# Kernel tuning notes

Hardware: AMD Instinct MI355X
Metric: run time of the kernel (lower is better)

Reference implementation:

```python
import jax, jax.numpy as jnp
import numpy as np

N, E, DIN, DOUT = 50000, 800000, 64, 64


def setup_inputs() -> dict:
    key = jax.random.key(0)
    k1, k2, k3, k4, k5 = jax.random.split(key, 5)
    x = jax.random.normal(k1, (N, DIN), dtype=jnp.float32)
    edge_index = jax.random.randint(k2, (2, E), 0, N, dtype=jnp.int64)
    edge_attr = jax.random.uniform(k3, (E,), dtype=jnp.float32)
    # PyG GCNConv params: linear weight (no bias in lin) + conv bias
    W = jax.random.normal(k4, (DIN, DOUT), dtype=jnp.float32) / np.sqrt(DIN)
    b = jax.random.normal(k5, (DOUT,), dtype=jnp.float32) * 0.01
    return {
        "x": x,
        "edge_index": edge_index,
        "edge_attr": edge_attr,
        "return_attention_weights": 0,
        "W": W,
        "b": b,
    }


def reference(x, edge_index, edge_attr, return_attention_weights, W, b):
    # GCNConv(add_self_loops=False, normalize=True), edge_weight = ones.
    # edge_attr / return_attention_weights are unused by the original module.
    n = x.shape[0]
    src, dst = edge_index[0], edge_index[1]
    # in-degree on destination nodes (gcn_norm with ones edge weights)
    deg = jax.ops.segment_sum(jnp.ones_like(src, dtype=x.dtype), dst, num_segments=n)
    dis = jnp.where(deg > 0, jax.lax.rsqrt(jnp.maximum(deg, 1)), jnp.zeros_like(deg))
    norm = dis[src] * dis[dst]  # [E]
    h = x @ W  # [N, DOUT] -- transform before aggregation (in < out would flip, equal here)
    msg = h[src] * norm[:, None]  # [E, DOUT]
    out = jax.ops.segment_sum(msg, dst, num_segments=n) + b  # [N, DOUT]
    return out
```

## Files before the change

### kernel.cpp

```cpp
#include <hip/hip_runtime.h>
#include <stdint.h>


#define CAP   64
#define BSH   7
#define NBMAX 512
#define EPB   4096
#define BCAP  2816

typedef float vf4 __attribute__((ext_vector_type(4)));

__device__ __forceinline__ int probe_is64(const void* eidx, int n_edges, int n_nodes) {
    int lane = threadIdx.x & 63;
    const long long* p = (const long long*)eidx;
    int cnt = n_edges < 64 ? n_edges : 64;
    long long v = p[lane % cnt];
    bool ok = (v >= 0) && (v < (long long)n_nodes);
    return (__ballot(ok) == ~0ull) ? 1 : 0;
}

__device__ __forceinline__ int load_idx(const void* eidx, long long i, int is64) {
    if (is64) return (int)((const long long*)eidx)[i];
    return ((const int*)eidx)[i];
}

__device__ __forceinline__ unsigned short f2bf(float v) {
    unsigned u = __float_as_uint(v);
    unsigned r = (u + 0x7fffu + ((u >> 16) & 1u)) >> 16;
    return (unsigned short)r;
}

__device__ __forceinline__ float bflo(unsigned u) { return __uint_as_float(u << 16); }
__device__ __forceinline__ float bfhi(unsigned u) { return __uint_as_float(u & 0xffff0000u); }

__global__ __launch_bounds__(256) void k_bin(
    const void* eidx, unsigned* __restrict__ tails,
    unsigned* __restrict__ buckets, int n, int ne, int nb)
{
    __shared__ unsigned histo[NBMAX];
    __shared__ unsigned base[NBMAX];
    const int tid = (int)threadIdx.x;
    for (int i = tid; i < NBMAX; i += 256) histo[i] = 0u;
    int is64 = probe_is64(eidx, ne, n);
    __syncthreads();

    unsigned pk[16], rk[16];
    long long e0 = (long long)blockIdx.x * EPB + tid;
    #pragma unroll
    for (int j = 0; j < 16; ++j) {
        long long e = e0 + 256 * j;
        if (e < (long long)ne) {
            int s = load_idx(eidx, e, is64);
            int t = load_idx(eidx, (long long)ne + e, is64);
            pk[j] = ((unsigned)t << 16) | (unsigned)s;
            rk[j] = atomicAdd(&histo[(unsigned)t >> BSH], 1u);
        } else { pk[j] = 0u; rk[j] = 0xFFFFFFFFu; }
    }
    __syncthreads();
    unsigned U = tails[NBMAX];
    for (int b2 = tid; b2 < nb; b2 += 256) {
        unsigned cc = histo[b2];
        base[b2] = cc ? (atomicAdd(&tails[b2], cc) - U) : 0u;
    }
    __syncthreads();
    #pragma unroll
    for (int j = 0; j < 16; ++j) {
        if (rk[j] != 0xFFFFFFFFu) {
            unsigned bk = pk[j] >> (16 + BSH);
            unsigned slot = base[bk] + rk[j];
            if (slot < (unsigned)BCAP)
                buckets[(size_t)bk * BCAP + slot] = pk[j];
        }
    }
}

__global__ __launch_bounds__(256) void k_gemm(
    const float* __restrict__ x, const float* __restrict__ W,
    unsigned* __restrict__ h32w, int n)
{
    __shared__ float Ws[64 * 64];
    __shared__ float xs[64 * 68];
    const int tid = (int)threadIdx.x;
    const int row0 = (int)blockIdx.x * 64;

    for (int j = 0; j < 4; ++j) {
        int q = tid + 256 * j;
        float4 w4 = ((const float4*)W)[q];
        float* d = &Ws[q * 4];
        d[0] = w4.x; d[1] = w4.y; d[2] = w4.z; d[3] = w4.w;
    }
    for (int j = 0; j < 4; ++j) {
        int q = tid + 256 * j;
        int r = q >> 4, c4 = (q & 15) * 4;
        int row = row0 + r;
        float4 v4 = (row < n) ? ((const float4*)x)[(size_t)row * 16 + (q & 15)]
                              : make_float4(0.f, 0.f, 0.f, 0.f);
        float* d = &xs[r * 68 + c4];
        d[0] = v4.x; d[1] = v4.y; d[2] = v4.z; d[3] = v4.w;
    }
    __syncthreads();

    const int fg = tid & 15, rg = tid >> 4;
    const int r0 = rg * 4;
    float acc[4][4];
    #pragma unroll
    for (int i = 0; i < 4; ++i)
        #pragma unroll
        for (int j = 0; j < 4; ++j) acc[i][j] = 0.f;

    #pragma unroll 4
    for (int k = 0; k < 64; ++k) {
        vf4 w4 = *(const vf4*)&Ws[k * 64 + fg * 4];
        float x0 = xs[(r0 + 0) * 68 + k];
        float x1 = xs[(r0 + 1) * 68 + k];
        float x2 = xs[(r0 + 2) * 68 + k];
        float x3 = xs[(r0 + 3) * 68 + k];
        acc[0][0] += x0 * w4.x; acc[0][1] += x0 * w4.y; acc[0][2] += x0 * w4.z; acc[0][3] += x0 * w4.w;
        acc[1][0] += x1 * w4.x; acc[1][1] += x1 * w4.y; acc[1][2] += x1 * w4.z; acc[1][3] += x1 * w4.w;
        acc[2][0] += x2 * w4.x; acc[2][1] += x2 * w4.y; acc[2][2] += x2 * w4.z; acc[2][3] += x2 * w4.w;
        acc[3][0] += x3 * w4.x; acc[3][1] += x3 * w4.y; acc[3][2] += x3 * w4.z; acc[3][3] += x3 * w4.w;
    }
    #pragma unroll
    for (int i = 0; i < 4; ++i) {
        int row = row0 + r0 + i;
        if (row < n) {
            h32w[(size_t)row * 32 + fg * 2] =
                (unsigned)f2bf(acc[i][0]) | ((unsigned)f2bf(acc[i][1]) << 16);
            h32w[(size_t)row * 32 + fg * 2 + 1] =
                (unsigned)f2bf(acc[i][2]) | ((unsigned)f2bf(acc[i][3]) << 16);
        }
    }
}

__global__ __launch_bounds__(256) void k_place2(
    const unsigned* __restrict__ tails,
    const unsigned* __restrict__ buckets,
    unsigned short* __restrict__ csr16,
    float* __restrict__ dis, unsigned char* __restrict__ endc, int n)
{
    __shared__ unsigned degL[1 << BSH];
    const int tid = (int)threadIdx.x;
    const int b = (int)blockIdx.x;
    const int t0 = b << BSH;
    if (tid < (1 << BSH)) degL[tid] = 0u;
    __syncthreads();
    unsigned U = tails[NBMAX];
    unsigned cnt = tails[b] - U;
    if (cnt > (unsigned)BCAP) cnt = (unsigned)BCAP;
    for (unsigned i = (unsigned)tid; i < cnt; i += 256) {
        unsigned p = buckets[(size_t)b * BCAP + i];
        unsigned dl = (p >> 16) & ((1u << BSH) - 1);
        unsigned r = atomicAdd(&degL[dl], 1u);
        if (r < (unsigned)CAP)
            csr16[((size_t)(t0 + (int)dl)) * CAP + r] = (unsigned short)(p & 0xFFFFu);
    }
    __syncthreads();
    if (tid < (1 << BSH)) {
        int node = t0 + tid;
        if (node < n) {
            unsigned d = degL[tid];
            dis[node] = d ? rsqrtf((float)d) : 0.f;
            endc[node] = (unsigned char)(d < (unsigned)CAP ? d : (unsigned)CAP);
        }
    }
}

__global__ __launch_bounds__(256) void k_place_direct(
    const void* eidx, unsigned* __restrict__ deg,
    unsigned short* __restrict__ csr16, int n, int ne)
{
    int is64 = probe_is64(eidx, ne, n);
    unsigned base = deg[n];
    int e = (int)blockIdx.x * 256 + (int)threadIdx.x;
    if (e >= ne) return;
    int s = load_idx(eidx, e, is64);
    int t = load_idx(eidx, (long long)ne + e, is64);
    unsigned r = atomicAdd(&deg[t], 1u) - base;
    if (r < (unsigned)CAP)
        csr16[(size_t)t * CAP + r] = (unsigned short)s;
}

__global__ __launch_bounds__(256) void k_finalize_direct(
    const unsigned* __restrict__ deg,
    float* __restrict__ dis, unsigned char* __restrict__ endc, int n)
{
    int i = (int)blockIdx.x * 256 + (int)threadIdx.x;
    if (i >= n) return;
    unsigned base = deg[n];
    unsigned cnt = deg[i] - base;
    dis[i] = cnt ? rsqrtf((float)cnt) : 0.f;
    endc[i] = (unsigned char)(cnt < (unsigned)CAP ? cnt : (unsigned)CAP);
}

__global__ __launch_bounds__(256) void k_aggregate(
    const float* __restrict__ dis,
    const unsigned char* __restrict__ endc,
    const unsigned short* __restrict__ csr16,
    const uint2* __restrict__ h64,
    const float* __restrict__ bias,
    float* __restrict__ out, int n)
{
    int wid  = (int)threadIdx.x >> 6;
    int lane = (int)threadIdx.x & 63;
    int t = (int)blockIdx.x * 4 + wid;
    if (t >= n) return;
    int allsrc = (int)csr16[(size_t)t * CAP + lane];
    unsigned end = endc[t];
    float dis_t = dis[t];
    int f = lane & 15, q = lane >> 4;
    float a0 = 0.f, a1 = 0.f, a2 = 0.f, a3 = 0.f;

    unsigned K4 = end >> 4;
    for (unsigned k = 0; k < K4; ++k) {
        int j = q + (int)(k << 4);
        int s0 = __shfl(allsrc, j, 64);
        int s1 = __shfl(allsrc, j + 4, 64);
        int s2 = __shfl(allsrc, j + 8, 64);
        int s3 = __shfl(allsrc, j + 12, 64);
        float w0 = dis[s0], w1 = dis[s1], w2 = dis[s2], w3 = dis[s3];
        uint2 u0 = h64[(size_t)s0 * 16 + f];
        uint2 u1 = h64[(size_t)s1 * 16 + f];
        uint2 u2 = h64[(size_t)s2 * 16 + f];
        uint2 u3 = h64[(size_t)s3 * 16 + f];
        a0 += w0 * bflo(u0.x) + w1 * bflo(u1.x) + w2 * bflo(u2.x) + w3 * bflo(u3.x);
        a1 += w0 * bfhi(u0.x) + w1 * bfhi(u1.x) + w2 * bfhi(u2.x) + w3 * bfhi(u3.x);
        a2 += w0 * bflo(u0.y) + w1 * bflo(u1.y) + w2 * bflo(u2.y) + w3 * bflo(u3.y);
        a3 += w0 * bfhi(u0.y) + w1 * bfhi(u1.y) + w2 * bfhi(u2.y) + w3 * bfhi(u3.y);
    }
    unsigned rem = end & 15u;
    if (rem) {
        unsigned jb = K4 << 4;
        for (unsigned k = 0; k < 4; ++k) {
            unsigned jj = jb + (k << 2) + (unsigned)q;
            bool valid = jj < end;
            int s = __shfl(allsrc, (int)(jj & 63u), 64);
            s = valid ? s : 0;
            float w = valid ? dis[s] : 0.f;
            uint2 u = h64[(size_t)s * 16 + f];
            a0 += w * bflo(u.x);
            a1 += w * bfhi(u.x);
            a2 += w * bflo(u.y);
            a3 += w * bfhi(u.y);
        }
    }
    a0 += __shfl_xor(a0, 16, 64); a0 += __shfl_xor(a0, 32, 64);
    a1 += __shfl_xor(a1, 16, 64); a1 += __shfl_xor(a1, 32, 64);
    a2 += __shfl_xor(a2, 16, 64); a2 += __shfl_xor(a2, 32, 64);
    a3 += __shfl_xor(a3, 16, 64); a3 += __shfl_xor(a3, 32, 64);
    if (q == 0) {
        float4 bb = ((const float4*)bias)[f];
        float4 o;
        o.x = a0 * dis_t + bb.x;
        o.y = a1 * dis_t + bb.y;
        o.z = a2 * dis_t + bb.z;
        o.w = a3 * dis_t + bb.w;
        ((float4*)out)[(size_t)t * 16 + f] = o;
    }
}

extern "C" void kernel_launch(void* const* d_in, const int* in_sizes, int n_in,
                              void* d_out, int out_size, void* d_ws, size_t ws_size,
                              hipStream_t stream) {
    const float* x   = (const float*)d_in[0];
    const void* eidx = d_in[1];
    const float* W   = (const float*)d_in[4];
    const float* b   = (const float*)d_in[5];
    float* out       = (float*)d_out;

    const int n  = in_sizes[0] / 64;
    const int ne = in_sizes[2];
    const int nb = (n + (1 << BSH) - 1) >> BSH;
    const int nchunks = (ne + EPB - 1) / EPB;

    auto al = [](size_t v) { return (v + 255) & ~(size_t)255; };

    size_t need = al((size_t)(NBMAX + 1) * 4) + al((size_t)nb * BCAP * 4)
                + al((size_t)n * CAP * 2) + al((size_t)n * 32 * 4)
                + al((size_t)n * 4) + al((size_t)n);
    bool binned = (ws_size >= need) && (nb <= NBMAX);

    char* base = (char*)d_ws;
    size_t off = 0;
    unsigned*       tails   = (unsigned*)(base + off);       off = al(off + (size_t)(NBMAX + 1) * 4);
    unsigned*       buckets = (unsigned*)(base + off);       off = al(off + (size_t)nb * BCAP * 4);
    unsigned short* csr16   = (unsigned short*)(base + off); off = al(off + (size_t)n * CAP * 2);
    unsigned*       h32     = (unsigned*)(base + off);       off = al(off + (size_t)n * 32 * 4);
    float*          dis     = (float*)(base + off);          off = al(off + (size_t)n * 4);
    unsigned char*  endc    = (unsigned char*)(base + off);  off = al(off + (size_t)n);

    if (binned) {
        k_bin<<<nchunks, 256, 0, stream>>>(eidx, tails, buckets, n, ne, nb);
        k_gemm<<<(n + 63) / 64, 256, 0, stream>>>(x, W, h32, n);
        k_place2<<<nb, 256, 0, stream>>>(tails, buckets, csr16, dis, endc, n);
    } else {
        unsigned* deg = buckets;
        k_gemm<<<(n + 63) / 64, 256, 0, stream>>>(x, W, h32, n);
        k_place_direct<<<(ne + 255) / 256, 256, 0, stream>>>(eidx, deg, csr16, n, ne);
        k_finalize_direct<<<(n + 255) / 256, 256, 0, stream>>>(deg, dis, endc, n);
    }
    k_aggregate<<<(n + 3) / 4, 256, 0, stream>>>(dis, endc, csr16, (const uint2*)h32, b, out, n);
}
```

Measured before the change: 125.3 us.

## Aggregate directly from dst buckets with LDS atomics, dropping CSR build

The binned path no longer builds a per-node CSR. A new k_deg kernel computes in-degree and dis per 64-node bucket, and k_agg2 streams each bucket's packed edges, gathers bf16 h rows and accumulates into a shared-memory 64x64 tile with float atomics before writing out with the bias. Bucket size shrinks from 128 to 64 nodes (NBMAX 1024, BCAP 1408), so there are more blocks and each has a smaller LDS tile. This removes the csr16 write and read and one kernel stage, at the cost of reading the buckets twice and doing many shared-memory float atomics, which may contend. It also drops the per-node cap of 64 neighbours. With N=50000 and 64-node buckets, nb is about 782, which stays under NBMAX 1024, so the binned path is still taken.

```diff
diff --git a/kernel.cpp b/kernel.cpp
--- a/kernel.cpp
+++ b/kernel.cpp
@@ -3,10 +3,10 @@
 
 
 #define CAP   64
-#define BSH   7
-#define NBMAX 512
+#define BSH   6
+#define NBMAX 1024
 #define EPB   4096
-#define BCAP  2816
+#define BCAP  1408
 
 typedef float vf4 __attribute__((ext_vector_type(4)));
 
@@ -74,6 +74,32 @@
     }
 }
 
+__global__ __launch_bounds__(256) void k_deg(
+    const unsigned* __restrict__ tails,
+    const unsigned* __restrict__ buckets,
+    float* __restrict__ dis, int n)
+{
+    __shared__ unsigned degL[1 << BSH];
+    const int tid = (int)threadIdx.x;
+    const int b = (int)blockIdx.x;
+    if (tid < (1 << BSH)) degL[tid] = 0u;
+    __syncthreads();
+    unsigned U = tails[NBMAX];
+    unsigned cnt = tails[b] - U;
+    if (cnt > (unsigned)BCAP) cnt = (unsigned)BCAP;
+    const size_t bbase = (size_t)b * BCAP;
+    for (unsigned i = (unsigned)tid; i < cnt; i += 256)
+        atomicAdd(&degL[(buckets[bbase + i] >> 16) & ((1u << BSH) - 1)], 1u);
+    __syncthreads();
+    if (tid < (1 << BSH)) {
+        int node = (b << BSH) + tid;
+        if (node < n) {
+            unsigned d = degL[tid];
+            dis[node] = d ? rsqrtf((float)d) : 0.f;
+        }
+    }
+}
+
 __global__ __launch_bounds__(256) void k_gemm(
     const float* __restrict__ x, const float* __restrict__ W,
     unsigned* __restrict__ h32w, int n)
@@ -132,35 +158,58 @@
     }
 }
 
-__global__ __launch_bounds__(256) void k_place2(
+__global__ __launch_bounds__(256) void k_agg2(
     const unsigned* __restrict__ tails,
     const unsigned* __restrict__ buckets,
-    unsigned short* __restrict__ csr16,
-    float* __restrict__ dis, unsigned char* __restrict__ endc, int n)
-{
-    __shared__ unsigned degL[1 << BSH];
+    const float* __restrict__ dis,
+    const uint2* __restrict__ h64,
+    const float* __restrict__ bias,
+    float* __restrict__ out, int n)
+{
+    __shared__ float accL[64 * 66];
     const int tid = (int)threadIdx.x;
     const int b = (int)blockIdx.x;
     const int t0 = b << BSH;
-    if (tid < (1 << BSH)) degL[tid] = 0u;
-    __syncthreads();
+    for (int i = tid; i < 64 * 66; i += 256) accL[i] = 0.f;
+    __syncthreads();
+
     unsigned U = tails[NBMAX];
     unsigned cnt = tails[b] - U;
     if (cnt > (unsigned)BCAP) cnt = (unsigned)BCAP;
-    for (unsigned i = (unsigned)tid; i < cnt; i += 256) {
-        unsigned p = buckets[(size_t)b * BCAP + i];
-        unsigned dl = (p >> 16) & ((1u << BSH) - 1);
-        unsigned r = atomicAdd(&degL[dl], 1u);
-        if (r < (unsigned)CAP)
-            csr16[((size_t)(t0 + (int)dl)) * CAP + r] = (unsigned short)(p & 0xFFFFu);
-    }
-    __syncthreads();
-    if (tid < (1 << BSH)) {
-        int node = t0 + tid;
+    const size_t bbase = (size_t)b * BCAP;
+
+    const int wid = tid >> 6, lane = tid & 63;
+    const int q = lane >> 4, f = lane & 15;
+    for (unsigned idx = (unsigned)(wid * 4 + q); idx < cnt; idx += 16) {
+        unsigned u = buckets[bbase + idx];
+        unsigned dl = (u >> 16) & ((1u << BSH) - 1);
+        unsigned src = u & 0xFFFFu;
+        float w = dis[src];
+        uint2 hv = h64[(size_t)src * 16 + f];
+        float* arow = &accL[dl * 66 + f * 4];
+        atomicAdd(&arow[0], w * bflo(hv.x));
+        atomicAdd(&arow[1], w * bfhi(hv.x));
+        atomicAdd(&arow[2], w * bflo(hv.y));
+        atomicAdd(&arow[3], w * bfhi(hv.y));
+    }
+    __syncthreads();
+
+    {
+        int r = tid >> 2, c = tid & 3;
+        int node = t0 + r;
         if (node < n) {
-            unsigned d = degL[tid];
-            dis[node] = d ? rsqrtf((float)d) : 0.f;
-            endc[node] = (unsigned char)(d < (unsigned)CAP ? d : (unsigned)CAP);
+            float dt = dis[node];
+            const float* arow = &accL[r * 66 + c * 16];
+            #pragma unroll
+            for (int k = 0; k < 4; ++k) {
+                float4 bb = ((const float4*)bias)[c * 4 + k];
+                vf4 o;
+                o.x = dt * arow[k * 4 + 0] + bb.x;
+                o.y = dt * arow[k * 4 + 1] + bb.y;
+                o.z = dt * arow[k * 4 + 2] + bb.z;
+                o.w = dt * arow[k * 4 + 3] + bb.w;
+                ((vf4*)out)[(size_t)node * 16 + c * 4 + k] = o;
+            }
         }
     }
 }
@@ -192,7 +241,7 @@
     endc[i] = (unsigned char)(cnt < (unsigned)CAP ? cnt : (unsigned)CAP);
 }
 
-__global__ __launch_bounds__(256) void k_aggregate(
+__global__ __launch_bounds__(256) void k_aggregate_csr(
     const float* __restrict__ dis,
     const unsigned char* __restrict__ endc,
     const unsigned short* __restrict__ csr16,
@@ -209,7 +258,6 @@
     float dis_t = dis[t];
     int f = lane & 15, q = lane >> 4;
     float a0 = 0.f, a1 = 0.f, a2 = 0.f, a3 = 0.f;
-
     unsigned K4 = end >> 4;
     for (unsigned k = 0; k < K4; ++k) {
         int j = q + (int)(k << 4);
@@ -275,28 +323,29 @@
     auto al = [](size_t v) { return (v + 255) & ~(size_t)255; };
 
     size_t need = al((size_t)(NBMAX + 1) * 4) + al((size_t)nb * BCAP * 4)
-                + al((size_t)n * CAP * 2) + al((size_t)n * 32 * 4)
-                + al((size_t)n * 4) + al((size_t)n);
+                + al((size_t)n * 32 * 4) + al((size_t)n * 4)
+                + al((size_t)n * CAP * 2) + al((size_t)n);
     bool binned = (ws_size >= need) && (nb <= NBMAX);
 
     char* base = (char*)d_ws;
     size_t off = 0;
     unsigned*       tails   = (unsigned*)(base + off);       off = al(off + (size_t)(NBMAX + 1) * 4);
     unsigned*       buckets = (unsigned*)(base + off);       off = al(off + (size_t)nb * BCAP * 4);
-    unsigned short* csr16   = (unsigned short*)(base + off); off = al(off + (size_t)n * CAP * 2);
     unsigned*       h32     = (unsigned*)(base + off);       off = al(off + (size_t)n * 32 * 4);
     float*          dis     = (float*)(base + off);          off = al(off + (size_t)n * 4);
+    unsigned short* csr16   = (unsigned short*)(base + off); off = al(off + (size_t)n * CAP * 2);
     unsigned char*  endc    = (unsigned char*)(base + off);  off = al(off + (size_t)n);
 
     if (binned) {
         k_bin<<<nchunks, 256, 0, stream>>>(eidx, tails, buckets, n, ne, nb);
+        k_deg<<<nb, 256, 0, stream>>>(tails, buckets, dis, n);
         k_gemm<<<(n + 63) / 64, 256, 0, stream>>>(x, W, h32, n);
-        k_place2<<<nb, 256, 0, stream>>>(tails, buckets, csr16, dis, endc, n);
+        k_agg2<<<nb, 256, 0, stream>>>(tails, buckets, dis, (const uint2*)h32, b, out, n);
     } else {
         unsigned* deg = buckets;
         k_gemm<<<(n + 63) / 64, 256, 0, stream>>>(x, W, h32, n);
         k_place_direct<<<(ne + 255) / 256, 256, 0, stream>>>(eidx, deg, csr16, n, ne);
         k_finalize_direct<<<(n + 255) / 256, 256, 0, stream>>>(deg, dis, endc, n);
-    }
-    k_aggregate<<<(n + 3) / 4, 256, 0, stream>>>(dis, endc, csr16, (const uint2*)h32, b, out, n);
-}
+        k_aggregate_csr<<<(n + 3) / 4, 256, 0, stream>>>(dis, endc, csr16, (const uint2*)h32, b, out, n);
+    }
+}
```

Measured after the change: 444.0 us. +254.4%, slower.
